# Kernel tuning notes

Hardware: AMD Instinct MI355X
Metric: run time of the kernel (lower is better)

## Reference

```python
import jax, jax.numpy as jnp
import numpy as np

FG_THR = 0.7
BG_THR = 0.3
NUM_PER_IMAGE = 256
NUM_POS_MAX = int(NUM_PER_IMAGE * 0.5)  # positive_ratio = 0.5
BBOX_W = (1.0, 1.0, 1.0, 1.0)
BETA = 1.0 / 9.0


def _permute(t, C):
    # N x (A*C) x H x W -> N x (H*W*A) x C, matching RPNLoss.permute
    N, _, H, W = t.shape
    t = t.reshape(N, -1, C, H, W)
    t = jnp.transpose(t, (0, 3, 4, 1, 2))
    return t.reshape(N, -1, C)


def _iou(a, b):
    # a: [N,4], b: [M,4] -> [N,M] (with +1 box convention, as in source)
    x_tl = jnp.maximum(a[:, None, 0], b[None, :, 0])
    y_tl = jnp.maximum(a[:, None, 1], b[None, :, 1])
    x_rb = jnp.minimum(a[:, None, 2], b[None, :, 2])
    y_rb = jnp.minimum(a[:, None, 3], b[None, :, 3])
    inter = jnp.clip(x_rb - x_tl + 1.0, 0.0) * jnp.clip(y_rb - y_tl + 1.0, 0.0)
    area1 = (a[:, 2] - a[:, 0] + 1.0) * (a[:, 3] - a[:, 1] + 1.0)
    area2 = (b[:, 2] - b[:, 0] + 1.0) * (b[:, 3] - b[:, 1] + 1.0)
    return inter / (area1[:, None] + area2[None, :] - inter)


def _encode(anchors, targets):
    ws = anchors[:, 2] - anchors[:, 0] + 1.0
    hs = anchors[:, 3] - anchors[:, 1] + 1.0
    x_ctr = anchors[:, 0] + 0.5 * ws
    y_ctr = anchors[:, 1] + 0.5 * hs
    t_ws = targets[:, 2] - targets[:, 0] + 1.0
    t_hs = targets[:, 3] - targets[:, 1] + 1.0
    t_x = targets[:, 0] + 0.5 * t_ws
    t_y = targets[:, 1] + 0.5 * t_hs
    wx, wy, ww, wh = BBOX_W
    tx = wx * (t_x - x_ctr) / ws
    ty = wy * (t_y - y_ctr) / hs
    tw = ww * jnp.log(t_ws / ws)
    th = wh * jnp.log(t_hs / hs)
    return jnp.stack([tx, ty, tw, th], axis=1)


def _bce_logits(l, t):
    return jnp.maximum(l, 0.0) - l * t + jnp.log1p(jnp.exp(-jnp.abs(l)))


def _per_image(anchor, logit, breg, size, target, key):
    N = anchor.shape[0]
    ious = _iou(anchor, target)  # [N, M]
    vals = ious.max(axis=1)
    ori = jnp.argmax(ious, axis=1).astype(jnp.int32)
    inds = jnp.where(vals < BG_THR, -1, ori)
    inds = jnp.where((vals >= BG_THR) & (vals < FG_THR), -2, inds)
    # low-quality matches: anchors achieving the per-target max IoU keep their argmax
    col_max = ious.max(axis=0)
    restore = (ious == col_max[None, :]).any(axis=1)
    inds = jnp.where(restore, ori, inds)
    # filter_anchors: keep anchors fully inside the image (size = (h, w))
    inside = (anchor[:, 0] >= 0) & (anchor[:, 1] >= 0) & \
             (anchor[:, 2] <= size[1] - 1.0) & (anchor[:, 3] <= size[0] - 1.0)
    inds = jnp.where(inside, inds, -2)

    pos = inds >= 0
    neg = inds == -1
    # random sampling via random priorities + fixed-size top_k with validity masks
    r = jax.random.uniform(key, (N,))
    pos_vals, pos_idx = jax.lax.top_k(jnp.where(pos, r, -1.0), NUM_POS_MAX)
    valid_pos = pos_vals >= 0.0
    num_pos = valid_pos.sum()
    neg_vals, neg_idx = jax.lax.top_k(jnp.where(neg, r, -1.0), NUM_PER_IMAGE)
    valid_neg = (neg_vals >= 0.0) & (jnp.arange(NUM_PER_IMAGE) < (NUM_PER_IMAGE - num_pos))

    # classification loss terms (BCE with logits); pos target 1, neg target 0
    vp = valid_pos.astype(logit.dtype)
    vn = valid_neg.astype(logit.dtype)
    cls_sum = jnp.sum(_bce_logits(logit[pos_idx], 1.0) * vp) + \
              jnp.sum(_bce_logits(logit[neg_idx], 0.0) * vn)
    count = num_pos + valid_neg.sum()

    m = jnp.clip(inds[pos_idx], 0, None)
    offsets = _encode(anchor[pos_idx], target[m])
    diff = jnp.abs(breg[pos_idx] - offsets)
    sl1 = jnp.where(diff < BETA, 0.5 * diff * diff / BETA, diff - 0.5 * BETA)
    reg_sum = jnp.sum(sl1 * vp[:, None])
    return cls_sum, count, reg_sum


def reference(anchors, logits, bbox_regs, sizes, targets):
    B = anchors.shape[0]
    log = _permute(logits, 1)[..., 0]      # [B, H*W*A]
    breg = _permute(bbox_regs, 4)          # [B, H*W*A, 4]
    keys = jax.random.split(jax.random.key(42), B)
    cls_s, cnt, reg_s = jax.vmap(_per_image)(anchors, log, breg, sizes, targets, keys)
    total = jnp.sum(cnt).astype(anchors.dtype)
    cls_loss = jnp.sum(cls_s) / total
    reg_loss = jnp.sum(reg_s) / total
    return jnp.stack([cls_loss, reg_loss])


def setup_inputs() -> dict:
    key = jax.random.key(0)
    ks = jax.random.split(key, 10)
    B, A, H, W, M = 4, 3, 168, 256, 32
    N = H * W * A
    IMG_H, IMG_W = 800.0, 1333.0
    x1 = jax.random.uniform(ks[0], (B, N)) * 1200.0
    y1 = jax.random.uniform(ks[1], (B, N)) * 700.0
    aw = jax.random.uniform(ks[2], (B, N)) * 300.0 + 16.0
    ah = jax.random.uniform(ks[3], (B, N)) * 300.0 + 16.0
    anchors = jnp.stack([x1, y1, x1 + aw, y1 + ah], axis=-1)  # some out of image -> filtered
    tx1 = jax.random.uniform(ks[4], (B, M)) * 1000.0
    ty1 = jax.random.uniform(ks[5], (B, M)) * 500.0
    tw = jax.random.uniform(ks[6], (B, M)) * 250.0 + 30.0
    th = jax.random.uniform(ks[7], (B, M)) * 200.0 + 30.0
    targets = jnp.stack([tx1, ty1, jnp.minimum(tx1 + tw, IMG_W - 1.0),
                         jnp.minimum(ty1 + th, IMG_H - 1.0)], axis=-1)
    logits = jax.random.normal(ks[8], (B, A, H, W), dtype=jnp.float32)
    bbox_regs = jax.random.normal(ks[9], (B, 4 * A, H, W), dtype=jnp.float32) * 0.1
    sizes = jnp.tile(jnp.array([IMG_H, IMG_W], dtype=jnp.float32), (B, 1))
    return {"anchors": anchors, "logits": logits, "bbox_regs": bbox_regs,
            "sizes": sizes, "targets": targets}
```

## Files before the change

kernel.cpp:

```cpp
#include <hip/hip_runtime.h>
#include <stdint.h>

#define Bn 4
#define An 3
#define Hn 168
#define Wn 256
#define Mn 32
#define HWn (Hn*Wn)
#define Nn (HWn*An)
#define POS_CAP 8192
#define BND_CAP 2048
#define NPERIM 256
#define NPOSMAX 128
#define FG_THR 0.7f
#define BG_THR 0.3f
#define BETA (1.0f/9.0f)

#define NBLK 126
#define APT 4
#define STRIDE (NBLK * 256)
#define SEG 1024

#define OFF_POSCNT 0
#define OFF_BNDCNT 4
#define OFF_BOUND  8
#define OFF_NEED   12
#define OFF_COUNT  16
#define OFF_CLS    17
#define OFF_REG    18
#define OFF_DONE   19
#define OFF_KEYS   24
#define OFF_PCM    32
#define OFF_NSEGC  16160
#define OFF_PHIST  16664
#define OFF_PLIST  532760
#define OFF_BLIST  598296
#define OFF_NLIST  614680

__device__ __forceinline__ uint32_t rotl32(uint32_t v, int n) { return (v << n) | (v >> (32 - n)); }

__device__ __forceinline__ void tf2x32(uint32_t k0, uint32_t k1, uint32_t x0, uint32_t x1,
                                       uint32_t& o0, uint32_t& o1) {
    uint32_t k2 = k0 ^ k1 ^ 0x1BD11BDAu;
    x0 += k0; x1 += k1;
    x0 += x1; x1 = rotl32(x1, 13); x1 ^= x0;
    x0 += x1; x1 = rotl32(x1, 15); x1 ^= x0;
    x0 += x1; x1 = rotl32(x1, 26); x1 ^= x0;
    x0 += x1; x1 = rotl32(x1, 6);  x1 ^= x0;
    x0 += k1; x1 += k2 + 1u;
    x0 += x1; x1 = rotl32(x1, 17); x1 ^= x0;
    x0 += x1; x1 = rotl32(x1, 29); x1 ^= x0;
    x0 += x1; x1 = rotl32(x1, 16); x1 ^= x0;
    x0 += x1; x1 = rotl32(x1, 24); x1 ^= x0;
    x0 += k2; x1 += k0 + 2u;
    x0 += x1; x1 = rotl32(x1, 13); x1 ^= x0;
    x0 += x1; x1 = rotl32(x1, 15); x1 ^= x0;
    x0 += x1; x1 = rotl32(x1, 26); x1 ^= x0;
    x0 += x1; x1 = rotl32(x1, 6);  x1 ^= x0;
    x0 += k0; x1 += k1 + 3u;
    x0 += x1; x1 = rotl32(x1, 17); x1 ^= x0;
    x0 += x1; x1 = rotl32(x1, 29); x1 ^= x0;
    x0 += x1; x1 = rotl32(x1, 16); x1 ^= x0;
    x0 += x1; x1 = rotl32(x1, 24); x1 ^= x0;
    x0 += k1; x1 += k2 + 4u;
    x0 += x1; x1 = rotl32(x1, 13); x1 ^= x0;
    x0 += x1; x1 = rotl32(x1, 15); x1 ^= x0;
    x0 += x1; x1 = rotl32(x1, 26); x1 ^= x0;
    x0 += x1; x1 = rotl32(x1, 6);  x1 ^= x0;
    x0 += k2; x1 += k0 + 5u;
    o0 = x0; o1 = x1;
}

__device__ __forceinline__ uint32_t rng_m23(uint32_t k0, uint32_t k1, uint32_t i) {
    uint32_t o0, o1;
    tf2x32(k0, k1, 0u, i, o0, o1);
    return (o0 ^ o1) >> 9;
}

__device__ __forceinline__ float iou_one(float a0, float a1, float a2, float a3,
                                         float t0, float t1, float t2, float t3) {
    float xtl = fmaxf(a0, t0), ytl = fmaxf(a1, t1);
    float xrb = fminf(a2, t2), yrb = fminf(a3, t3);
    float iw = fmaxf(xrb - xtl + 1.0f, 0.0f);
    float ih = fmaxf(yrb - ytl + 1.0f, 0.0f);
    float inter = iw * ih;
    float area1 = (a2 - a0 + 1.0f) * (a3 - a1 + 1.0f);
    float area2 = (t2 - t0 + 1.0f) * (t3 - t1 + 1.0f);
    return inter * __builtin_amdgcn_rcpf(area1 + area2 - inter);
}

__global__ void __launch_bounds__(256) k1_colmax(const float* __restrict__ anchors,
                                                 const float* __restrict__ targets,
                                                 uint32_t* __restrict__ ws) {
    int b = blockIdx.y, j = blockIdx.x, tid = threadIdx.x;
    if (b == 0 && j == 0) {
        if (tid < 24) ws[tid] = 0u;
        if (tid == 0) {
            for (int bb = 0; bb < Bn; ++bb) {
                uint32_t o0, o1;
                tf2x32(0u, 42u, 0u, (uint32_t)bb, o0, o1);
                ws[OFF_KEYS + 2*bb] = o0; ws[OFF_KEYS + 2*bb + 1] = o1;
            }
        }
    }
    __shared__ float part[4][Mn];
    int base = j * 256 + tid;
    float4 a[APT];
    #pragma unroll
    for (int k = 0; k < APT; ++k)
        a[k] = ((const float4*)anchors)[b * Nn + base + k * STRIDE];
    float cm[Mn];
    #pragma unroll 4
    for (int t = 0; t < Mn; ++t) {
        float4 tv = ((const float4*)targets)[b * Mn + t];
        float m0 = 0.0f;
        #pragma unroll
        for (int k = 0; k < APT; ++k)
            m0 = fmaxf(m0, iou_one(a[k].x, a[k].y, a[k].z, a[k].w, tv.x, tv.y, tv.z, tv.w));
        cm[t] = m0;
    }
    #pragma unroll
    for (int t = 0; t < Mn; ++t) {
        #pragma unroll
        for (int o = 32; o > 0; o >>= 1) cm[t] = fmaxf(cm[t], __shfl_xor(cm[t], o, 64));
    }
    int wid = tid >> 6, lane = tid & 63;
    if (lane == 0) {
        #pragma unroll
        for (int t = 0; t < Mn; ++t) part[wid][t] = cm[t];
    }
    __syncthreads();
    if (tid < Mn) {
        float v = fmaxf(fmaxf(part[0][tid], part[1][tid]),
                        fmaxf(part[2][tid], part[3][tid]));
        ws[OFF_PCM + ((size_t)b * NBLK + j) * Mn + tid] = __float_as_uint(v);
    }
}

__global__ void __launch_bounds__(256) k2_cat(const float* __restrict__ anchors,
                                              const float* __restrict__ targets,
                                              const float* __restrict__ sizes,
                                              uint32_t* __restrict__ ws) {
    int b = blockIdx.y, j = blockIdx.x, tid = threadIdx.x;
    __shared__ float cmf[Mn];
    __shared__ float redf[256];
    __shared__ uint32_t lh[1024];
    __shared__ uint32_t segcnt;
    {
        int t = tid & 31, sub = tid >> 5;
        float acc = 0.0f;
        for (int jj = sub; jj < NBLK; jj += 8)
            acc = fmaxf(acc, __uint_as_float(ws[OFF_PCM + ((size_t)b * NBLK + jj) * Mn + t]));
        redf[tid] = acc;
        __syncthreads();
        if (sub == 0) {
            #pragma unroll
            for (int q = 1; q < 8; ++q) acc = fmaxf(acc, redf[t + 32 * q]);
            cmf[t] = acc;
        }
    }
    #pragma unroll
    for (int q = 0; q < 4; ++q) lh[tid + 256 * q] = 0u;
    if (tid == 0) segcnt = 0u;
    __syncthreads();

    int base = j * 256 + tid;
    float4 av[APT];
    #pragma unroll
    for (int k = 0; k < APT; ++k)
        av[k] = ((const float4*)anchors)[b * Nn + base + k * STRIDE];
    float rowmax[APT]; int ori[APT]; bool restore[APT];
    #pragma unroll
    for (int k = 0; k < APT; ++k) { rowmax[k] = -1.0f; ori[k] = 0; restore[k] = false; }
    #pragma unroll 4
    for (int t = 0; t < Mn; ++t) {
        float4 tv = ((const float4*)targets)[b * Mn + t];
        float cmv = cmf[t];
        #pragma unroll
        for (int k = 0; k < APT; ++k) {
            float iou = iou_one(av[k].x, av[k].y, av[k].z, av[k].w, tv.x, tv.y, tv.z, tv.w);
            if (iou > rowmax[k]) { rowmax[k] = iou; ori[k] = t; }
            restore[k] = restore[k] || (iou == cmv);
        }
    }
    float sh = sizes[b * 2 + 0], sw = sizes[b * 2 + 1];
    uint32_t key0 = ws[OFF_KEYS + 2 * b], key1 = ws[OFF_KEYS + 2 * b + 1];
    int lane = tid & 63;
    unsigned long long lt_mask = (lane == 63) ? 0x7FFFFFFFFFFFFFFFull : ((1ull << lane) - 1ull);
    uint2* nseg = (uint2*)(ws + OFF_NLIST) + (size_t)(b * NBLK + j) * SEG;
    #pragma unroll
    for (int k = 0; k < APT; ++k) {
        int i = base + k * STRIDE;
        bool inside = (av[k].x >= 0.0f) && (av[k].y >= 0.0f) &&
                      (av[k].z <= sw - 1.0f) && (av[k].w <= sh - 1.0f);
        uint32_t cat = 0;
        if (inside) {
            if (restore[k] || rowmax[k] >= FG_THR) cat = 2;
            else if (rowmax[k] < BG_THR) cat = 1;
        }
        uint32_t m = rng_m23(key0, key1, (uint32_t)i);
        unsigned long long pmask = __ballot(cat == 2u);
        if (pmask) {
            int leader = __ffsll((long long)pmask) - 1;
            uint32_t bb = 0;
            if (lane == leader) bb = atomicAdd(&ws[OFF_POSCNT + b], (uint32_t)__popcll(pmask));
            bb = __shfl(bb, leader, 64);
            if (cat == 2u) {
                uint32_t p = bb + (uint32_t)__popcll(pmask & lt_mask);
                if (p < POS_CAP)
                    ((uint2*)(ws + OFF_PLIST))[(size_t)b * POS_CAP + p] =
                        make_uint2(m, (uint32_t)i | ((uint32_t)ori[k] << 17));
            }
        }
        unsigned long long nmask = __ballot(cat == 1u);
        if (nmask) {
            int leader = __ffsll((long long)nmask) - 1;
            uint32_t bb = 0;
            if (lane == leader) bb = atomicAdd(&segcnt, (uint32_t)__popcll(nmask));
            bb = __shfl(bb, leader, 64);
            if (cat == 1u) {
                uint32_t p = bb + (uint32_t)__popcll(nmask & lt_mask);
                nseg[p] = make_uint2(m, (uint32_t)i);
                atomicAdd(&lh[m >> 13], 1u);
            }
        }
    }
    __syncthreads();
    uint32_t* slice = ws + OFF_PHIST + ((size_t)b * NBLK + j) * 1024;
    #pragma unroll
    for (int q = 0; q < 4; ++q) slice[tid + 256 * q] = lh[tid + 256 * q];
    if (tid == 0) ws[OFF_NSEGC + b * NBLK + j] = segcnt;
}

__global__ void __launch_bounds__(256) k25_bound(uint32_t* __restrict__ ws) {
    int b = blockIdx.x, t = threadIdx.x;
    __shared__ uint32_t csum[256];
    uint4 h = make_uint4(0, 0, 0, 0);
    const uint32_t* ph = ws + OFF_PHIST + (size_t)b * NBLK * 1024;
    for (int s = 0; s < NBLK; ++s) {
        uint4 v = ((const uint4*)(ph + (size_t)s * 1024))[t];
        h.x += v.x; h.y += v.y; h.z += v.z; h.w += v.w;
    }
    uint32_t sum = h.x + h.y + h.z + h.w;
    csum[t] = sum;
    __syncthreads();
    for (int off = 1; off < 256; off <<= 1) {
        uint32_t mine = csum[t];
        uint32_t add = (t + off < 256) ? csum[t + off] : 0u;
        __syncthreads();
        csum[t] = mine + add;
        __syncthreads();
    }
    uint32_t pc = ws[OFF_POSCNT + b];
    int num_pos = (pc < (uint32_t)NPOSMAX) ? (int)pc : NPOSMAX;
    int k_neg = NPERIM - num_pos;
    uint32_t total = csum[0];
    if ((int)total < k_neg) {
        if (t == 0) {
            ws[OFF_BOUND + b] = 0xFFFFFFFFu;
            ws[OFF_NEED + b] = 0u;
            atomicAdd(&ws[OFF_COUNT], (uint32_t)(num_pos + (int)total));
        }
        return;
    }
    uint32_t incl = csum[t];
    uint32_t next = (t < 255) ? csum[t + 1] : 0u;
    if ((int)incl >= k_neg && (int)next < k_neg) {
        int cum = (int)next;
        uint32_t hv[4] = { h.x, h.y, h.z, h.w };
        int boundary = -1, needed = 0;
        #pragma unroll
        for (int q = 3; q >= 0; --q) {
            int c = (int)hv[q];
            if (cum + c >= k_neg) { boundary = 4 * t + q; needed = k_neg - cum; break; }
            cum += c;
        }
        ws[OFF_BOUND + b] = (uint32_t)boundary;
        ws[OFF_NEED + b] = (uint32_t)needed;
        atomicAdd(&ws[OFF_COUNT], (uint32_t)(num_pos + k_neg));
    }
}

__global__ void __launch_bounds__(256) k3_neg(const float* __restrict__ logits,
                                              uint32_t* __restrict__ ws) {
    int b = blockIdx.y, j = blockIdx.x;
    int bd = (int)(int32_t)ws[OFF_BOUND + b];
    int cnt = (int)ws[OFF_NSEGC + b * NBLK + j];
    const uint2* nseg = (const uint2*)(ws + OFF_NLIST) + (size_t)(b * NBLK + j) * SEG;
    float local = 0.0f;
    for (int idx = (int)threadIdx.x; idx < cnt; idx += 256) {
        uint2 e = nseg[idx];
        int bk = (int)(e.x >> 13);
        if (bk > bd) {
            int i = (int)e.y;
            int a = i % An, hw = i / An;
            float l = logits[(b * An + a) * HWn + hw];
            local += fmaxf(l, 0.0f) + log1pf(expf(-fabsf(l)));
        } else if (bk == bd) {
            uint32_t q = atomicAdd(&ws[OFF_BNDCNT + b], 1u);
            if (q < BND_CAP)
                ((uint2*)(ws + OFF_BLIST))[(size_t)b * BND_CAP + q] = e;
        }
    }
    __shared__ float red[256];
    red[threadIdx.x] = local;
    __syncthreads();
    for (int s = 128; s > 0; s >>= 1) {
        if ((int)threadIdx.x < s) red[threadIdx.x] += red[threadIdx.x + s];
        __syncthreads();
    }
    if (threadIdx.x == 0 && red[0] != 0.0f) atomicAdd((float*)&ws[OFF_CLS], red[0]);
}

__device__ __forceinline__ bool sel_less(uint2 a, uint2 b) {
    return (a.x > b.x) || (a.x == b.x && a.y < b.y);
}

__device__ void bitonic_sort_shared(uint2* buf, int n) {
    for (int k = 2; k <= n; k <<= 1) {
        for (int j = k >> 1; j > 0; j >>= 1) {
            for (int t = (int)threadIdx.x; t < n; t += 256) {
                int ixj = t ^ j;
                if (ixj > t) {
                    uint2 x = buf[t], y = buf[ixj];
                    bool up = ((t & k) == 0);
                    bool sw = up ? sel_less(y, x) : sel_less(x, y);
                    if (sw) { buf[t] = y; buf[ixj] = x; }
                }
            }
            __syncthreads();
        }
    }
}

__global__ void __launch_bounds__(256) k4_final(const float* __restrict__ anchors,
                                                const float* __restrict__ targets,
                                                const float* __restrict__ logits,
                                                const float* __restrict__ bregs,
                                                uint32_t* __restrict__ ws,
                                                float* __restrict__ out) {
    int b = blockIdx.x, tid = threadIdx.x;
    __shared__ uint2 buf[BND_CAP];
    __shared__ float red[256];
    float cls = 0.0f, reg = 0.0f;

    uint32_t pcu = ws[OFF_POSCNT + b];
    int pc = (pcu < (uint32_t)POS_CAP) ? (int)pcu : POS_CAP;
    const uint2* plist = (const uint2*)(ws + OFF_PLIST) + (size_t)b * POS_CAP;
    int psel = (pc < NPOSMAX) ? pc : NPOSMAX;
    bool use_buf = false;
    if (pc > NPOSMAX) {
        int n = (pc < BND_CAP) ? pc : BND_CAP;
        for (int t = tid; t < n; t += 256) buf[t] = plist[t];
        int npad = 1; while (npad < n) npad <<= 1;
        for (int t = tid; t < npad; t += 256) if (t >= n) buf[t] = make_uint2(0u, 0xFFFFFFFFu);
        __syncthreads();
        bitonic_sort_shared(buf, npad);
        use_buf = true;
        psel = (NPOSMAX < n) ? NPOSMAX : n;
    }
    for (int t = tid; t < psel; t += 256) {
        uint32_t packed = use_buf ? buf[t].y : plist[t].y;
        int i = (int)(packed & 0x1FFFFu);
        int ori = (int)(packed >> 17);
        int a = i % An, hw = i / An;
        float l = logits[(b * An + a) * HWn + hw];
        cls += fmaxf(l, 0.0f) - l + log1pf(expf(-fabsf(l)));
        float4 av = ((const float4*)anchors)[b * Nn + i];
        float4 tv = ((const float4*)targets)[b * Mn + ori];
        float aws = av.z - av.x + 1.0f, ahs = av.w - av.y + 1.0f;
        float axc = av.x + 0.5f * aws, ayc = av.y + 0.5f * ahs;
        float tws = tv.z - tv.x + 1.0f, ths = tv.w - tv.y + 1.0f;
        float txc = tv.x + 0.5f * tws, tyc = tv.y + 0.5f * ths;
        float off0 = (txc - axc) / aws;
        float off1 = (tyc - ayc) / ahs;
        float off2 = logf(tws / aws);
        float off3 = logf(ths / ahs);
        float br0 = bregs[(b * 12 + a * 4 + 0) * HWn + hw];
        float br1 = bregs[(b * 12 + a * 4 + 1) * HWn + hw];
        float br2 = bregs[(b * 12 + a * 4 + 2) * HWn + hw];
        float br3 = bregs[(b * 12 + a * 4 + 3) * HWn + hw];
        float d;
        d = fabsf(br0 - off0); reg += (d < BETA) ? 0.5f * d * d / BETA : d - 0.5f * BETA;
        d = fabsf(br1 - off1); reg += (d < BETA) ? 0.5f * d * d / BETA : d - 0.5f * BETA;
        d = fabsf(br2 - off2); reg += (d < BETA) ? 0.5f * d * d / BETA : d - 0.5f * BETA;
        d = fabsf(br3 - off3); reg += (d < BETA) ? 0.5f * d * d / BETA : d - 0.5f * BETA;
    }
    __syncthreads();

    int need = (int)ws[OFF_NEED + b];
    if (need > 0) {
        uint32_t nbu = ws[OFF_BNDCNT + b];
        int nb = (nbu < (uint32_t)BND_CAP) ? (int)nbu : BND_CAP;
        const uint2* blist = (const uint2*)(ws + OFF_BLIST) + (size_t)b * BND_CAP;
        for (int t = tid; t < nb; t += 256) buf[t] = blist[t];
        int npad = 1; while (npad < nb) npad <<= 1;
        for (int t = tid; t < npad; t += 256) if (t >= nb) buf[t] = make_uint2(0u, 0xFFFFFFFFu);
        __syncthreads();
        bitonic_sort_shared(buf, npad);
        int sel = (need < nb) ? need : nb;
        for (int t = tid; t < sel; t += 256) {
            int i = (int)buf[t].y;
            int a = i % An, hw = i / An;
            float l = logits[(b * An + a) * HWn + hw];
            cls += fmaxf(l, 0.0f) + log1pf(expf(-fabsf(l)));
        }
    }

    red[tid] = cls;
    __syncthreads();
    for (int s = 128; s > 0; s >>= 1) {
        if (tid < s) red[tid] += red[tid + s];
        __syncthreads();
    }
    if (tid == 0 && red[0] != 0.0f) atomicAdd((float*)&ws[OFF_CLS], red[0]);
    __syncthreads();
    red[tid] = reg;
    __syncthreads();
    for (int s = 128; s > 0; s >>= 1) {
        if (tid < s) red[tid] += red[tid + s];
        __syncthreads();
    }
    if (tid == 0) {
        if (red[0] != 0.0f) atomicAdd((float*)&ws[OFF_REG], red[0]);
        __threadfence();
        uint32_t old = atomicAdd(&ws[OFF_DONE], 1u);
        if (old == Bn - 1) {
            float cls_tot = __uint_as_float(atomicAdd(&ws[OFF_CLS], 0u));
            float reg_tot = __uint_as_float(atomicAdd(&ws[OFF_REG], 0u));
            float cnt = (float)atomicAdd(&ws[OFF_COUNT], 0u);
            out[0] = cls_tot / cnt;
            out[1] = reg_tot / cnt;
        }
    }
}

extern "C" void kernel_launch(void* const* d_in, const int* in_sizes, int n_in,
                              void* d_out, int out_size, void* d_ws, size_t ws_size,
                              hipStream_t stream) {
    const float* anchors = (const float*)d_in[0];
    const float* logits  = (const float*)d_in[1];
    const float* bregs   = (const float*)d_in[2];
    const float* sizes   = (const float*)d_in[3];
    const float* targets = (const float*)d_in[4];
    float* out = (float*)d_out;
    uint32_t* ws = (uint32_t*)d_ws;

    k1_colmax<<<dim3(NBLK, Bn), dim3(256), 0, stream>>>(anchors, targets, ws);
    k2_cat<<<dim3(NBLK, Bn), dim3(256), 0, stream>>>(anchors, targets, sizes, ws);
    k25_bound<<<dim3(Bn), dim3(256), 0, stream>>>(ws);
    k3_neg<<<dim3(NBLK, Bn), dim3(256), 0, stream>>>(logits, ws);
    k4_final<<<dim3(Bn), dim3(256), 0, stream>>>(anchors, targets, logits, bregs, ws, out);
}
```

Measured before the change: 157.0 us.

## Compute IoU once in k1 and pass per-anchor equality masks to k2

k1 now computes each anchor's row max, argmax, inside flag, thresholds and a 32-bit mask of which targets hit the per-wave column max, stores them packed, and writes per-wave column maxima. k2 no longer recomputes the 32-target IoU. It combines the wave maxima into the global column max, builds a per-wave mask of targets whose global max lies in that wave, and ANDs that with the stored masks to find restore anchors. This removes the second IoU pass. In exchange each anchor writes and reads an 8-byte packed record, and the column-max reduction grows to four times as many partials.

```diff
diff --git a/kernel.cpp b/kernel.cpp
--- a/kernel.cpp
+++ b/kernel.cpp
@@ -20,6 +20,7 @@
 #define APT 4
 #define STRIDE (NBLK * 256)
 #define SEG 1024
+#define WPI (NBLK * 4)
 
 #define OFF_POSCNT 0
 #define OFF_BNDCNT 4
@@ -30,12 +31,13 @@
 #define OFF_REG    18
 #define OFF_DONE   19
 #define OFF_KEYS   24
-#define OFF_PCM    32
-#define OFF_NSEGC  16160
-#define OFF_PHIST  16664
-#define OFF_PLIST  532760
-#define OFF_BLIST  598296
-#define OFF_NLIST  614680
+#define OFF_WMAX   32
+#define OFF_PACKED 64544
+#define OFF_NSEGC  1096736
+#define OFF_PHIST  1097240
+#define OFF_PLIST  1613336
+#define OFF_BLIST  1678872
+#define OFF_NLIST  1695256
 
 __device__ __forceinline__ uint32_t rotl32(uint32_t v, int n) { return (v << n) | (v >> (32 - n)); }
 
@@ -91,6 +93,7 @@
 
 __global__ void __launch_bounds__(256) k1_colmax(const float* __restrict__ anchors,
                                                  const float* __restrict__ targets,
+                                                 const float* __restrict__ sizes,
                                                  uint32_t* __restrict__ ws) {
     int b = blockIdx.y, j = blockIdx.x, tid = threadIdx.x;
     if (b == 0 && j == 0) {
@@ -103,45 +106,54 @@
             }
         }
     }
-    __shared__ float part[4][Mn];
+    int lane = tid & 63;
+    int w = j * 4 + (tid >> 6);
     int base = j * 256 + tid;
     float4 a[APT];
     #pragma unroll
     for (int k = 0; k < APT; ++k)
         a[k] = ((const float4*)anchors)[b * Nn + base + k * STRIDE];
-    float cm[Mn];
+    float rowmax[APT]; int ori[APT]; uint32_t eqm[APT];
+    #pragma unroll
+    for (int k = 0; k < APT; ++k) { rowmax[k] = -1.0f; ori[k] = 0; eqm[k] = 0u; }
+    float mywm = 0.0f;
     #pragma unroll 4
     for (int t = 0; t < Mn; ++t) {
         float4 tv = ((const float4*)targets)[b * Mn + t];
+        float iou[APT];
         float m0 = 0.0f;
         #pragma unroll
+        for (int k = 0; k < APT; ++k) {
+            iou[k] = iou_one(a[k].x, a[k].y, a[k].z, a[k].w, tv.x, tv.y, tv.z, tv.w);
+            if (iou[k] > rowmax[k]) { rowmax[k] = iou[k]; ori[k] = t; }
+            m0 = fmaxf(m0, iou[k]);
+        }
+        #pragma unroll
+        for (int o = 32; o > 0; o >>= 1) m0 = fmaxf(m0, __shfl_xor(m0, o, 64));
+        #pragma unroll
         for (int k = 0; k < APT; ++k)
-            m0 = fmaxf(m0, iou_one(a[k].x, a[k].y, a[k].z, a[k].w, tv.x, tv.y, tv.z, tv.w));
-        cm[t] = m0;
-    }
-    #pragma unroll
-    for (int t = 0; t < Mn; ++t) {
-        #pragma unroll
-        for (int o = 32; o > 0; o >>= 1) cm[t] = fmaxf(cm[t], __shfl_xor(cm[t], o, 64));
-    }
-    int wid = tid >> 6, lane = tid & 63;
-    if (lane == 0) {
-        #pragma unroll
-        for (int t = 0; t < Mn; ++t) part[wid][t] = cm[t];
-    }
-    __syncthreads();
-    if (tid < Mn) {
-        float v = fmaxf(fmaxf(part[0][tid], part[1][tid]),
-                        fmaxf(part[2][tid], part[3][tid]));
-        ws[OFF_PCM + ((size_t)b * NBLK + j) * Mn + tid] = __float_as_uint(v);
-    }
-}
-
-__global__ void __launch_bounds__(256) k2_cat(const float* __restrict__ anchors,
-                                              const float* __restrict__ targets,
-                                              const float* __restrict__ sizes,
-                                              uint32_t* __restrict__ ws) {
+            eqm[k] |= (iou[k] == m0) ? (1u << t) : 0u;
+        mywm = (lane == t) ? m0 : mywm;
+    }
+    if (lane < Mn)
+        ws[OFF_WMAX + ((size_t)b * WPI + w) * Mn + lane] = __float_as_uint(mywm);
+    float sh = sizes[b * 2 + 0], sw = sizes[b * 2 + 1];
+    #pragma unroll
+    for (int k = 0; k < APT; ++k) {
+        int i = base + k * STRIDE;
+        uint32_t inside = (a[k].x >= 0.0f) && (a[k].y >= 0.0f) &&
+                          (a[k].z <= sw - 1.0f) && (a[k].w <= sh - 1.0f);
+        uint32_t flags = (uint32_t)ori[k] | (inside << 5) |
+                         ((rowmax[k] >= FG_THR ? 1u : 0u) << 6) |
+                         ((rowmax[k] <  BG_THR ? 1u : 0u) << 7);
+        ((uint2*)(ws + OFF_PACKED))[(size_t)b * Nn + i] = make_uint2(eqm[k], flags);
+    }
+}
+
+__global__ void __launch_bounds__(256) k2_cat(uint32_t* __restrict__ ws) {
     int b = blockIdx.y, j = blockIdx.x, tid = threadIdx.x;
+    int lane = tid & 63;
+    int w = j * 4 + (tid >> 6);
     __shared__ float cmf[Mn];
     __shared__ float redf[256];
     __shared__ uint32_t lh[1024];
@@ -149,8 +161,8 @@
     {
         int t = tid & 31, sub = tid >> 5;
         float acc = 0.0f;
-        for (int jj = sub; jj < NBLK; jj += 8)
-            acc = fmaxf(acc, __uint_as_float(ws[OFF_PCM + ((size_t)b * NBLK + jj) * Mn + t]));
+        for (int ww = sub; ww < WPI; ww += 8)
+            acc = fmaxf(acc, __uint_as_float(ws[OFF_WMAX + ((size_t)b * WPI + ww) * Mn + t]));
         redf[tid] = acc;
         __syncthreads();
         if (sub == 0) {
@@ -163,40 +175,28 @@
     for (int q = 0; q < 4; ++q) lh[tid + 256 * q] = 0u;
     if (tid == 0) segcnt = 0u;
     __syncthreads();
-
-    int base = j * 256 + tid;
-    float4 av[APT];
-    #pragma unroll
-    for (int k = 0; k < APT; ++k)
-        av[k] = ((const float4*)anchors)[b * Nn + base + k * STRIDE];
-    float rowmax[APT]; int ori[APT]; bool restore[APT];
-    #pragma unroll
-    for (int k = 0; k < APT; ++k) { rowmax[k] = -1.0f; ori[k] = 0; restore[k] = false; }
-    #pragma unroll 4
-    for (int t = 0; t < Mn; ++t) {
-        float4 tv = ((const float4*)targets)[b * Mn + t];
-        float cmv = cmf[t];
-        #pragma unroll
-        for (int k = 0; k < APT; ++k) {
-            float iou = iou_one(av[k].x, av[k].y, av[k].z, av[k].w, tv.x, tv.y, tv.z, tv.w);
-            if (iou > rowmax[k]) { rowmax[k] = iou; ori[k] = t; }
-            restore[k] = restore[k] || (iou == cmv);
-        }
-    }
-    float sh = sizes[b * 2 + 0], sw = sizes[b * 2 + 1];
+    float wmv = (lane < Mn)
+        ? __uint_as_float(ws[OFF_WMAX + ((size_t)b * WPI + w) * Mn + lane]) : -1.0f;
+    float cmv = (lane < Mn) ? cmf[lane] : 0.0f;
+    uint32_t gmask = (uint32_t)__ballot(lane < Mn && wmv == cmv);
+
     uint32_t key0 = ws[OFF_KEYS + 2 * b], key1 = ws[OFF_KEYS + 2 * b + 1];
-    int lane = tid & 63;
     unsigned long long lt_mask = (lane == 63) ? 0x7FFFFFFFFFFFFFFFull : ((1ull << lane) - 1ull);
     uint2* nseg = (uint2*)(ws + OFF_NLIST) + (size_t)(b * NBLK + j) * SEG;
+    int base = j * 256 + tid;
     #pragma unroll
     for (int k = 0; k < APT; ++k) {
         int i = base + k * STRIDE;
-        bool inside = (av[k].x >= 0.0f) && (av[k].y >= 0.0f) &&
-                      (av[k].z <= sw - 1.0f) && (av[k].w <= sh - 1.0f);
+        uint2 pk = ((const uint2*)(ws + OFF_PACKED))[(size_t)b * Nn + i];
+        uint32_t ori = pk.y & 31u;
+        bool inside = (pk.y >> 5) & 1u;
+        bool gefg   = (pk.y >> 6) & 1u;
+        bool ltbg   = (pk.y >> 7) & 1u;
+        bool restore = (pk.x & gmask) != 0u;
         uint32_t cat = 0;
         if (inside) {
-            if (restore[k] || rowmax[k] >= FG_THR) cat = 2;
-            else if (rowmax[k] < BG_THR) cat = 1;
+            if (restore || gefg) cat = 2;
+            else if (ltbg) cat = 1;
         }
         uint32_t m = rng_m23(key0, key1, (uint32_t)i);
         unsigned long long pmask = __ballot(cat == 2u);
@@ -209,7 +209,7 @@
                 uint32_t p = bb + (uint32_t)__popcll(pmask & lt_mask);
                 if (p < POS_CAP)
                     ((uint2*)(ws + OFF_PLIST))[(size_t)b * POS_CAP + p] =
-                        make_uint2(m, (uint32_t)i | ((uint32_t)ori[k] << 17));
+                        make_uint2(m, (uint32_t)i | (ori << 17));
             }
         }
         unsigned long long nmask = __ballot(cat == 1u);
@@ -446,8 +446,8 @@
     float* out = (float*)d_out;
     uint32_t* ws = (uint32_t*)d_ws;
 
-    k1_colmax<<<dim3(NBLK, Bn), dim3(256), 0, stream>>>(anchors, targets, ws);
-    k2_cat<<<dim3(NBLK, Bn), dim3(256), 0, stream>>>(anchors, targets, sizes, ws);
+    k1_colmax<<<dim3(NBLK, Bn), dim3(256), 0, stream>>>(anchors, targets, sizes, ws);
+    k2_cat<<<dim3(NBLK, Bn), dim3(256), 0, stream>>>(ws);
     k25_bound<<<dim3(Bn), dim3(256), 0, stream>>>(ws);
     k3_neg<<<dim3(NBLK, Bn), dim3(256), 0, stream>>>(logits, ws);
     k4_final<<<dim3(Bn), dim3(256), 0, stream>>>(anchors, targets, logits, bregs, ws, out);
```

New measurement: 161.6 us. 1.03x slower.
